# Performance work log

Hardware: AMD Instinct MI355X
Metric: run time of the kernel (lower is better)

## Reference

```python
import jax, jax.numpy as jnp
import numpy as np

CL = 256   # context_length (global in original code)
IL = 64    # inst_length (global in original code)
PC, CH1, CH2, CH3 = 64, 128, 256, 256
CK1, CK2, CK3 = 3, 3, 3
CS1, CS2, CS3 = 1, 2, 2
CP1, CP2, CP3 = 1, 1, 1
BCH1, BCH2, BCH3 = 64, 128, 256
F1, OUT = 1024, 2
B = 2048
C3_OUT = 64 * CH3            # 16384, per __init__ formula with CL-1=255
F1_IN = C3_OUT + BCH3        # 16640


def _conv1d(x, W, b, stride, pad):
    # x: [B, Cin, L], W: [Cout, Cin, K]
    y = jax.lax.conv_general_dilated(x, W, window_strides=(stride,),
                                     padding=[(pad, pad)],
                                     dimension_numbers=("NCH", "OIH", "NCH"))
    return y + b[None, :, None]


def setup_inputs() -> dict:
    key = jax.random.key(0)
    ks = jax.random.split(key, 20)
    s = lambda *sh: 1.0 / np.sqrt(np.prod(sh[1:]))
    def w(k, *sh):
        return jax.random.normal(k, sh, dtype=jnp.float32) * s(*sh)
    return {
        "x": jax.random.normal(ks[0], (B, CL * IL), dtype=jnp.float32),
        "Wp": w(ks[1], PC, IL, 2), "bp": jnp.zeros((PC,), jnp.float32),
        "W1": w(ks[2], CH1, PC, CK1), "b1": jnp.zeros((CH1,), jnp.float32),
        "W2": w(ks[3], CH2, CH1, CK2), "b2": jnp.zeros((CH2,), jnp.float32),
        "W3": w(ks[4], CH3, CH2, CK3), "b3": jnp.zeros((CH3,), jnp.float32),
        "Wb1": w(ks[5], BCH1, IL), "bb1": jnp.zeros((BCH1,), jnp.float32),
        "Wb2": w(ks[6], BCH2, BCH1), "bb2": jnp.zeros((BCH2,), jnp.float32),
        "Wb3": w(ks[7], BCH3, BCH2), "bb3": jnp.zeros((BCH3,), jnp.float32),
        "Wfc1": w(ks[8], F1, F1_IN), "bfc1": jnp.zeros((F1,), jnp.float32),
        "Wfc2": w(ks[9], OUT, F1), "bfc2": jnp.zeros((OUT,), jnp.float32),
    }


def reference(x, Wp, bp, W1, b1, W2, b2, W3, b3,
              Wb1, bb1, Wb2, bb2, Wb3, bb3, Wfc1, bfc1, Wfc2, bfc2):
    xr = x.reshape(-1, CL, IL).transpose(0, 2, 1)   # [B, IL, CL]
    x0 = xr[:, :, 0]                                 # [B, IL]
    # Fused replacement for the convp loop: kernel-2 conv over (x0, x_i)
    # y[:, :, i-1] = Wp[:,:,0] @ x0 + Wp[:,:,1] @ x_i + bp
    y = (jnp.einsum("bi,pi->bp", x0, Wp[:, :, 0])[:, :, None]
         + jnp.einsum("bic,pi->bpc", xr[:, :, 1:], Wp[:, :, 1])
         + bp[None, :, None])                        # [B, PC, CL-1]
    # bypass path on the first instruction (kernel-size-1 convs == matmuls)
    f = jax.nn.relu(x0 @ Wb1.T + bb1)
    f = jax.nn.relu(f @ Wb2.T + bb2)
    f = jax.nn.relu(f @ Wb3.T + bb3)                 # [B, BCH3]
    h = jax.nn.relu(y)
    h = jax.nn.relu(_conv1d(h, W1, b1, CS1, CP1))
    h = jax.nn.relu(_conv1d(h, W2, b2, CS2, CP2))
    h = jax.nn.relu(_conv1d(h, W3, b3, CS3, CP3))    # [B, CH3, 64]
    h = h.reshape(h.shape[0], C3_OUT)
    z = jnp.concatenate([h, f], axis=1)              # [B, F1_IN]
    z = jax.nn.relu(z @ Wfc1.T + bfc1)
    return z @ Wfc2.T + bfc2                         # [B, OUT]
```

## Files before the change

kernel.cpp:

```cpp
#include <hip/hip_runtime.h>
#include <cstdint>
#include <cstddef>

typedef __attribute__((ext_vector_type(8))) short bf16x8;
typedef __attribute__((ext_vector_type(8))) unsigned short ushort8;
typedef __attribute__((ext_vector_type(4))) float f32x4;

__device__ __forceinline__ unsigned short f2bf(float f){
  unsigned int u = __float_as_uint(f);
  unsigned int lsb = (u >> 16) & 1u;
  u += 0x7fffu + lsb;
  return (unsigned short)(u >> 16);
}

__device__ __forceinline__ void gload16(const void* g, void* l){
  __builtin_amdgcn_global_load_lds(
      (const __attribute__((address_space(1))) unsigned int*)g,
      (__attribute__((address_space(3))) unsigned int*)l, 16, 0, 0);
}

__global__ __launch_bounds__(256) void pack_w_bf16_kernel(const float* __restrict__ W,
                                                          unsigned short* __restrict__ Wb,
                                                          int COUT, int CIN){
  int idx = blockIdx.x*256 + threadIdx.x;
  int tot = COUT*CIN*3;
  if (idx >= tot) return;
  int o = idx/(CIN*3); int r = idx - o*(CIN*3); int kk = r/CIN; int ci = r - kk*CIN;
  Wb[idx] = f2bf(W[(o*CIN + ci)*3 + kk]);
}

__global__ __launch_bounds__(256) void pack_wp_kernel(const float* __restrict__ Wp,
                                                      unsigned short* __restrict__ Bw){
  int idx = blockIdx.x*256 + threadIdx.x;
  if (idx >= 64*128) return;
  int p = idx >> 7, k = idx & 127;
  float v = (k < 64) ? Wp[p*128 + k*2] : Wp[p*128 + (k-64)*2 + 1];
  Bw[idx] = f2bf(v);
}

__global__ __launch_bounds__(256) void f2bf_kernel(const float* __restrict__ src,
                                                   unsigned short* __restrict__ dst, int n){
  int i = blockIdx.x*256 + threadIdx.x;
  if (i < n) dst[i] = f2bf(src[i]);
}

__global__ __launch_bounds__(256) void zero_guards_kernel(unsigned short* __restrict__ buf,
                                                          int LINP, int CIN, int nb){
  int idx = blockIdx.x*256 + threadIdx.x;
  int per = 2*CIN/8;
  if (idx >= nb*per) return;
  int b = idx / per, r = idx - b*per;
  int g = r / (CIN/8), c8 = r - g*(CIN/8);
  ushort8 z = {0,0,0,0,0,0,0,0};
  *(ushort8*)(buf + ((size_t)b*LINP + (size_t)g*(LINP-1))*CIN + c8*8) = z;
}

__global__ __launch_bounds__(256) void branch_kernel(const float* __restrict__ x,
    const float* __restrict__ Wb1, const float* __restrict__ bb1,
    const float* __restrict__ Wb2, const float* __restrict__ bb2,
    const float* __restrict__ Wb3, const float* __restrict__ bb3,
    unsigned short* __restrict__ Hcat){
  __shared__ float s0[64], s1[64], s2[128];
  const int b = blockIdx.x, tid = threadIdx.x;
  const float* xb = x + (size_t)b*16384;
  if (tid < 64) s0[tid] = xb[tid];
  __syncthreads();
  if (tid < 64){
    float a = bb1[tid];
    for (int k=0;k<64;k++) a = fmaf(Wb1[tid*64+k], s0[k], a);
    s1[tid] = fmaxf(a, 0.f);
  }
  __syncthreads();
  if (tid < 128){
    float a = bb2[tid];
    for (int k=0;k<64;k++) a = fmaf(Wb2[tid*64+k], s1[k], a);
    s2[tid] = fmaxf(a, 0.f);
  }
  __syncthreads();
  float a = bb3[tid];
  for (int k=0;k<128;k++) a = fmaf(Wb3[tid*128+k], s2[k], a);
  Hcat[(size_t)b*16640 + 16384 + tid] = f2bf(fmaxf(a, 0.f));
}

__global__ __launch_bounds__(256) void h0_gemm_kernel(const float* __restrict__ x,
    const unsigned short* __restrict__ Bw, const float* __restrict__ bp,
    unsigned short* __restrict__ h0o){
  __shared__ __align__(16) char sAraw[128*256];
  __shared__ __align__(16) char sBraw[64*256];
  const int tid = threadIdx.x;
  const int m0 = blockIdx.x*128;
  #pragma unroll
  for (int i=0;i<16;i++){
    int j = tid + 256*i;
    int row = j >> 5, q = j & 31;
    int m = m0 + row;
    int b = m / 255, c = m - b*255;
    const float* xb = x + (size_t)b*16384;
    int k = q*4;
    const float* src = (k < 64) ? (xb + k) : (xb + (c+1)*64 + (k-64));
    float4 v = *(const float4*)src;
    ushort4 u; u.x=f2bf(v.x); u.y=f2bf(v.y); u.z=f2bf(v.z); u.w=f2bf(v.w);
    *(ushort4*)(sAraw + row*256 + ((k*2) ^ ((row&7)<<4))) = u;
  }
  #pragma unroll
  for (int i=0;i<4;i++){
    int j = tid + 256*i;
    int row = j >> 4, q = j & 15;
    int k = q*8;
    ushort8 u = *(const ushort8*)(Bw + row*128 + k);
    *(ushort8*)(sBraw + row*256 + ((k*2) ^ ((row&7)<<4))) = u;
  }
  __syncthreads();
  const int lane = tid & 63, wid = tid >> 6;
  const int lr = lane & 15, lg = lane >> 4;
  f32x4 zero = {0.f,0.f,0.f,0.f};
  f32x4 acc[2][4];
  #pragma unroll
  for (int a=0;a<2;a++){ acc[a][0]=zero; acc[a][1]=zero; acc[a][2]=zero; acc[a][3]=zero; }
  #pragma unroll
  for (int ks=0; ks<4; ks++){
    int k = ks*32 + lg*8;
    bf16x8 af[2], bfr[4];
    #pragma unroll
    for (int f=0; f<2; f++){
      int row = wid*32 + f*16 + lr;
      af[f] = *(const bf16x8*)(sAraw + row*256 + ((k*2) ^ ((row&7)<<4)));
    }
    #pragma unroll
    for (int f=0; f<4; f++){
      int row = f*16 + lr;
      bfr[f] = *(const bf16x8*)(sBraw + row*256 + ((k*2) ^ ((row&7)<<4)));
    }
    #pragma unroll
    for (int fi=0; fi<2; fi++)
      #pragma unroll
      for (int fj=0; fj<4; fj++)
        acc[fi][fj] = __builtin_amdgcn_mfma_f32_16x16x32_bf16(af[fi], bfr[fj], acc[fi][fj], 0,0,0);
  }
  #pragma unroll
  for (int fi=0; fi<2; fi++)
    #pragma unroll
    for (int fj=0; fj<4; fj++)
      #pragma unroll
      for (int j=0;j<4;j++){
        int m = m0 + wid*32 + fi*16 + lg*4 + j;
        int n = fj*16 + lr;
        int b = m / 255, t = m - b*255;
        h0o[((size_t)b*257 + t + 1)*64 + n] = f2bf(fmaxf(acc[fi][fj][j] + bp[n], 0.f));
      }
}

template<int CIN,int COUT,int S,int LINP,int LOUT,bool TO_HCAT>
__global__ __launch_bounds__(256) void conv_gemm_kernel(
    const unsigned short* __restrict__ in, const unsigned short* __restrict__ Wb,
    const float* __restrict__ bias, unsigned short* __restrict__ out){
  constexpr int K = 3*CIN;
  constexpr int KS = K/64;
  __shared__ __align__(16) char sA[128*128];
  __shared__ __align__(16) char sB[128*128];
  const int tid = threadIdx.x;
  const int m0 = blockIdx.x*128;
  const int n0 = blockIdx.y*128;
  const int lane = tid & 63, wid = tid >> 6;
  const int wm = wid >> 1, wn = wid & 1;
  const int lr = lane & 15, lg = lane >> 4;
  const int srow = lane >> 3;
  const int soff = (((lane&7) ^ srow) << 3);
  const unsigned short* abase[4];
  const unsigned short* bbase[4];
  #pragma unroll
  for (int s=0;s<4;s++){
    int row = wid*32 + s*8 + srow;
    int m = m0 + row;
    int b = m / LOUT, t = m - b*LOUT;
    abase[s] = in + ((size_t)b*LINP + (size_t)t*S)*CIN + soff;
    bbase[s] = Wb + (size_t)(n0+row)*K + soff;
  }
  f32x4 zero = {0.f,0.f,0.f,0.f};
  f32x4 acc[4][4];
  #pragma unroll
  for (int i=0;i<4;i++){ acc[i][0]=zero; acc[i][1]=zero; acc[i][2]=zero; acc[i][3]=zero; }
  for (int ks=0; ks<KS; ks++){
    const int k0 = ks*64;
    __syncthreads();
    #pragma unroll
    for (int s=0;s<4;s++){
      gload16(abase[s] + k0, sA + wid*4096 + s*1024);
      gload16(bbase[s] + k0, sB + wid*4096 + s*1024);
    }
    __syncthreads();
    #pragma unroll
    for (int kss=0; kss<2; kss++){
      const int k = kss*32 + lg*8;
      bf16x8 af[4], bfr[4];
      #pragma unroll
      for (int f=0;f<4;f++){
        int ra = wm*64 + f*16 + lr;
        af[f]  = *(const bf16x8*)(sA + ra*128 + ((k*2) ^ ((ra&7)<<4)));
        int rb = wn*64 + f*16 + lr;
        bfr[f] = *(const bf16x8*)(sB + rb*128 + ((k*2) ^ ((rb&7)<<4)));
      }
      #pragma unroll
      for (int fi=0;fi<4;fi++)
        #pragma unroll
        for (int fj=0;fj<4;fj++)
          acc[fi][fj] = __builtin_amdgcn_mfma_f32_16x16x32_bf16(af[fi], bfr[fj], acc[fi][fj], 0,0,0);
    }
  }
  #pragma unroll
  for (int fi=0;fi<4;fi++)
    #pragma unroll
    for (int fj=0;fj<4;fj++)
      #pragma unroll
      for (int j=0;j<4;j++){
        int m = m0 + wm*64 + fi*16 + lg*4 + j;
        int n = n0 + wn*64 + fj*16 + lr;
        int b = m / LOUT, t = m - b*LOUT;
        float val = fmaxf(acc[fi][fj][j] + bias[n], 0.f);
        if (TO_HCAT) out[(size_t)b*16640 + (size_t)n*64 + t] = f2bf(val);
        else         out[((size_t)b*(LOUT+2) + t + 1)*COUT + n] = f2bf(val);
      }
}

__global__ __launch_bounds__(256) void fc1_gemm_kernel(
    const unsigned short* __restrict__ A, const unsigned short* __restrict__ Bw,
    float* __restrict__ zp, int zoffm, int MT, int KZ){
  __shared__ __align__(16) char sA[128*128];
  __shared__ __align__(16) char sB[128*128];
  const int tid = threadIdx.x;
  const int nwg = gridDim.x;
  const int lgid = (blockIdx.x % 8)*(nwg/8) + blockIdx.x/8;
  const int kz  = lgid / (8*MT);
  const int rem = lgid % (8*MT);
  const int nt  = rem / MT;
  const int mt  = rem % MT;
  const int n0 = nt*128, m0 = mt*128;
  const int lane = tid & 63, wid = tid >> 6;
  const int wm = wid >> 1, wn = wid & 1;
  const int lr = lane & 15, lg = lane >> 4;
  const int srow = lane >> 3;
  const int soff = (((lane&7) ^ srow) << 3);
  f32x4 zero = {0.f,0.f,0.f,0.f};
  f32x4 acc[4][4];
  #pragma unroll
  for (int i=0;i<4;i++){ acc[i][0]=zero; acc[i][1]=zero; acc[i][2]=zero; acc[i][3]=zero; }
  const int it0 = (kz*260)/KZ, it1 = ((kz+1)*260)/KZ;
  for (int it=it0; it<it1; ++it){
    const size_t k0 = (size_t)it*64;
    __syncthreads();
    #pragma unroll
    for (int s=0;s<4;s++){
      int row = wid*32 + s*8 + srow;
      gload16(A  + (size_t)(m0+row)*16640 + k0 + soff, sA + wid*4096 + s*1024);
      gload16(Bw + (size_t)(n0+row)*16640 + k0 + soff, sB + wid*4096 + s*1024);
    }
    __syncthreads();
    #pragma unroll
    for (int ks=0; ks<2; ks++){
      const int k = ks*32 + lg*8;
      bf16x8 af[4], bfr[4];
      #pragma unroll
      for (int f=0;f<4;f++){
        int rowa = wm*64 + f*16 + lr;
        af[f]  = *(const bf16x8*)(sA + rowa*128 + ((k*2) ^ ((rowa&7)<<4)));
        int rowb = wn*64 + f*16 + lr;
        bfr[f] = *(const bf16x8*)(sB + rowb*128 + ((k*2) ^ ((rowb&7)<<4)));
      }
      #pragma unroll
      for (int fi=0;fi<4;fi++)
        #pragma unroll
        for (int fj=0;fj<4;fj++)
          acc[fi][fj] = __builtin_amdgcn_mfma_f32_16x16x32_bf16(af[fi], bfr[fj], acc[fi][fj], 0,0,0);
    }
  }
  float* zo = zp + (size_t)kz*zoffm;
  #pragma unroll
  for (int fi=0;fi<4;fi++)
    #pragma unroll
    for (int fj=0;fj<4;fj++)
      #pragma unroll
      for (int j=0;j<4;j++){
        int m = m0 + wm*64 + fi*16 + lg*4 + j;
        int n = n0 + wn*64 + fj*16 + lr;
        zo[(size_t)m*1024 + n] = acc[fi][fj][j];
      }
}

__global__ __launch_bounds__(256) void fc2_kernel(const float* __restrict__ zp, int zoffm, int KZ,
    const float* __restrict__ bfc1, const float* __restrict__ Wfc2,
    const float* __restrict__ bfc2, float* __restrict__ out){
  __shared__ float red[4][2];
  const int b = blockIdx.x, tid = threadIdx.x;
  float a0 = 0.f, a1 = 0.f;
  for (int n = tid; n < 1024; n += 256){
    float s = bfc1[n];
    const float* zb = zp + (size_t)b*1024 + n;
    for (int kz = 0; kz < KZ; kz++) s += zb[(size_t)kz*zoffm];
    s = fmaxf(s, 0.f);
    a0 = fmaf(s, Wfc2[n], a0);
    a1 = fmaf(s, Wfc2[1024+n], a1);
  }
  #pragma unroll
  for (int m=32; m>=1; m>>=1){ a0 += __shfl_xor(a0, m, 64); a1 += __shfl_xor(a1, m, 64); }
  const int w = tid >> 6;
  if ((tid & 63) == 0){ red[w][0] = a0; red[w][1] = a1; }
  __syncthreads();
  if (tid == 0){
    float s0 = red[0][0]+red[1][0]+red[2][0]+red[3][0];
    float s1 = red[0][1]+red[1][1]+red[2][1]+red[3][1];
    out[(size_t)b*2]   = s0 + bfc2[0];
    out[(size_t)b*2+1] = s1 + bfc2[1];
  }
}

extern "C" void kernel_launch(void* const* d_in, const int* in_sizes, int n_in,
                              void* d_out, int out_size, void* d_ws, size_t ws_size,
                              hipStream_t stream){
  const float* x    = (const float*)d_in[0];
  const float* Wp   = (const float*)d_in[1];
  const float* bp   = (const float*)d_in[2];
  const float* W1   = (const float*)d_in[3];
  const float* b1   = (const float*)d_in[4];
  const float* W2   = (const float*)d_in[5];
  const float* b2   = (const float*)d_in[6];
  const float* W3   = (const float*)d_in[7];
  const float* b3   = (const float*)d_in[8];
  const float* Wb1  = (const float*)d_in[9];
  const float* bb1  = (const float*)d_in[10];
  const float* Wb2  = (const float*)d_in[11];
  const float* bb2  = (const float*)d_in[12];
  const float* Wb3  = (const float*)d_in[13];
  const float* bb3  = (const float*)d_in[14];
  const float* Wfc1 = (const float*)d_in[15];
  const float* bfc1 = (const float*)d_in[16];
  const float* Wfc2 = (const float*)d_in[17];
  const float* bfc2 = (const float*)d_in[18];
  float* out = (float*)d_out;

  size_t off = 0;
  char* basep = (char*)d_ws;
  auto carve = [&](size_t bytes)->char*{
    char* q = basep + off; off += (bytes + 255) & ~(size_t)255; return q;
  };
  unsigned short* W1b   = (unsigned short*)carve((size_t)128*3*64*2);
  unsigned short* W2b   = (unsigned short*)carve((size_t)256*3*128*2);
  unsigned short* W3b   = (unsigned short*)carve((size_t)256*3*256*2);
  unsigned short* Bwp   = (unsigned short*)carve((size_t)64*128*2);
  unsigned short* Wfc1b = (unsigned short*)carve((size_t)1024*16640*2);
  size_t fixed = off;

  int Bc = 128, KZ = 64;
  {
    const int bcs[5] = {2048, 1024, 512, 256, 128};
    const int kzs[5] = {4, 8, 16, 32, 64};
    for (int i = 0; i < 5; i++){
      size_t b = bcs[i];
      size_t need = fixed + b*((size_t)66560+65792+33280) + (size_t)kzs[i]*b*4096 + 16*256;
      if (need <= ws_size){ Bc = bcs[i]; KZ = kzs[i]; break; }
    }
  }
  const int NC = 2048/Bc;
  const int MT = Bc/128;
  unsigned short* buf1 = (unsigned short*)carve((size_t)Bc*66560);
  unsigned short* buf2 = (unsigned short*)carve((size_t)Bc*65792);
  unsigned short* Hcat = (unsigned short*)carve((size_t)Bc*33280);
  float*          zp   = (float*)carve((size_t)KZ*Bc*4096);
  const int zoffm = Bc*1024;

  hipLaunchKernelGGL(pack_w_bf16_kernel, dim3((128*64*3+255)/256), dim3(256), 0, stream, W1, W1b, 128, 64);
  hipLaunchKernelGGL(pack_w_bf16_kernel, dim3((256*128*3+255)/256), dim3(256), 0, stream, W2, W2b, 256, 128);
  hipLaunchKernelGGL(pack_w_bf16_kernel, dim3((256*256*3+255)/256), dim3(256), 0, stream, W3, W3b, 256, 256);
  hipLaunchKernelGGL(pack_wp_kernel, dim3(32), dim3(256), 0, stream, Wp, Bwp);
  hipLaunchKernelGGL(f2bf_kernel, dim3((17039360+255)/256), dim3(256), 0, stream, Wfc1, Wfc1b, 17039360);

  for (int c = 0; c < NC; ++c){
    const float* xc = x + (size_t)c*Bc*16384;
    hipLaunchKernelGGL(zero_guards_kernel, dim3((Bc*2*64/8+255)/256), dim3(256), 0, stream,
                       buf1, 257, 64, Bc);
    hipLaunchKernelGGL(zero_guards_kernel, dim3((Bc*2*128/8+255)/256), dim3(256), 0, stream,
                       buf2, 257, 128, Bc);
    hipLaunchKernelGGL(branch_kernel, dim3(Bc), dim3(256), 0, stream,
                       xc, Wb1, bb1, Wb2, bb2, Wb3, bb3, Hcat);
    hipLaunchKernelGGL(h0_gemm_kernel, dim3(Bc*255/128), dim3(256), 0, stream, xc, Bwp, bp, buf1);
    hipLaunchKernelGGL((conv_gemm_kernel<64,128,1,257,255,false>), dim3(Bc*255/128, 1), dim3(256), 0, stream,
                       buf1, W1b, b1, buf2);
    hipLaunchKernelGGL(zero_guards_kernel, dim3((Bc*2*256/8+255)/256), dim3(256), 0, stream,
                       buf1, 130, 256, Bc);
    hipLaunchKernelGGL((conv_gemm_kernel<128,256,2,257,128,false>), dim3(Bc, 2), dim3(256), 0, stream,
                       buf2, W2b, b2, buf1);
    hipLaunchKernelGGL((conv_gemm_kernel<256,256,2,130,64,true>), dim3(Bc/2, 2), dim3(256), 0, stream,
                       buf1, W3b, b3, Hcat);
    hipLaunchKernelGGL(fc1_gemm_kernel, dim3(8*MT*KZ), dim3(256), 0, stream,
                       Hcat, Wfc1b, zp, zoffm, MT, KZ);
    hipLaunchKernelGGL(fc2_kernel, dim3(Bc), dim3(256), 0, stream,
                       zp, zoffm, KZ, bfc1, Wfc2, bfc2, out + (size_t)c*Bc*2);
  }
}
```

Measured before the change: 554.8 us.

## Replace conv im2col GEMM with per-sample slab-staged conv kernels

The three conv layers now load a contiguous slab of input rows for one sample into LDS once and reuse it across the three kernel taps, instead of re-gathering an im2col-style A tile for every K chunk. Weight tiles are double-buffered so the next chunk's load overlaps the current MFMAs, and a swizzled block index remaps workgroups. Buffers are split into separate h0/c1/c2 areas so all guard zeroing happens up front. The trade-off is smaller M tiles for conv2 and conv3 (64 and 32 rows), which lowers MFMA work per block and adds more blocks.

```diff
diff --git a/kernel.cpp b/kernel.cpp
--- a/kernel.cpp
+++ b/kernel.cpp
@@ -20,8 +20,7 @@
 }
 
 __global__ __launch_bounds__(256) void pack_w_bf16_kernel(const float* __restrict__ W,
-                                                          unsigned short* __restrict__ Wb,
-                                                          int COUT, int CIN){
+    unsigned short* __restrict__ Wb, int COUT, int CIN){
   int idx = blockIdx.x*256 + threadIdx.x;
   int tot = COUT*CIN*3;
   if (idx >= tot) return;
@@ -113,10 +112,11 @@
   __syncthreads();
   const int lane = tid & 63, wid = tid >> 6;
   const int lr = lane & 15, lg = lane >> 4;
-  f32x4 zero = {0.f,0.f,0.f,0.f};
   f32x4 acc[2][4];
   #pragma unroll
-  for (int a=0;a<2;a++){ acc[a][0]=zero; acc[a][1]=zero; acc[a][2]=zero; acc[a][3]=zero; }
+  for (int a=0;a<2;a++)
+    #pragma unroll
+    for (int j=0;j<4;j++) acc[a][j] = (f32x4){0,0,0,0};
   #pragma unroll
   for (int ks=0; ks<4; ks++){
     int k = ks*32 + lg*8;
@@ -150,75 +150,109 @@
       }
 }
 
-template<int CIN,int COUT,int S,int LINP,int LOUT,bool TO_HCAT>
-__global__ __launch_bounds__(256) void conv_gemm_kernel(
+template<int CIN,int COUT,int S,int LOUT,int PADIN,int PADOUT,int BM,int MPB,int MF,bool TO_HCAT>
+__global__ __launch_bounds__(256) void conv_slab_kernel(
     const unsigned short* __restrict__ in, const unsigned short* __restrict__ Wb,
     const float* __restrict__ bias, unsigned short* __restrict__ out){
-  constexpr int K = 3*CIN;
-  constexpr int KS = K/64;
-  __shared__ __align__(16) char sA[128*128];
-  __shared__ __align__(16) char sB[128*128];
-  const int tid = threadIdx.x;
-  const int m0 = blockIdx.x*128;
-  const int n0 = blockIdx.y*128;
-  const int lane = tid & 63, wid = tid >> 6;
-  const int wm = wid >> 1, wn = wid & 1;
-  const int lr = lane & 15, lg = lane >> 4;
-  const int srow = lane >> 3;
-  const int soff = (((lane&7) ^ srow) << 3);
-  const unsigned short* abase[4];
-  const unsigned short* bbase[4];
-  #pragma unroll
-  for (int s=0;s<4;s++){
-    int row = wid*32 + s*8 + srow;
-    int m = m0 + row;
-    int b = m / LOUT, t = m - b*LOUT;
-    abase[s] = in + ((size_t)b*LINP + (size_t)t*S)*CIN + soff;
-    bbase[s] = Wb + (size_t)(n0+row)*K + soff;
-  }
-  f32x4 zero = {0.f,0.f,0.f,0.f};
-  f32x4 acc[4][4];
-  #pragma unroll
-  for (int i=0;i<4;i++){ acc[i][0]=zero; acc[i][1]=zero; acc[i][2]=zero; acc[i][3]=zero; }
-  for (int ks=0; ks<KS; ks++){
-    const int k0 = ks*64;
-    __syncthreads();
+  constexpr int NT   = COUT/128;
+  constexpr int NCH  = 3*CIN/64;
+  constexpr int CP8  = CIN/8;
+  constexpr int CB   = CIN*2;
+  constexpr int SROWS = 2048/CP8;
+  constexpr int LDSROWS = SROWS + 4;
+  __shared__ __align__(16) char S_[LDSROWS*CB + 32768];
+  char* SA = S_;
+  char* SB = S_ + LDSROWS*CB;
+
+  const int tid = threadIdx.x, lane = tid & 63, wv = tid >> 6;
+  const int nwg = gridDim.x;
+  const int bid = blockIdx.x;
+  const int lgid = (bid & 7)*(nwg >> 3) + (bid >> 3);
+  const int nt  = lgid % NT;
+  const int mtb = lgid / NT;
+  const int mt  = mtb % MPB;
+  const int b   = mtb / MPB;
+  const int n0  = nt*128;
+  const int t0  = mt*BM;
+  const unsigned short* Ab = in + ((size_t)b*PADIN + (size_t)t0*S)*CIN;
+
+  #pragma unroll
+  for (int i=0;i<8;i++){
+    int slot = (wv*8+i)*64 + lane;
+    int row = slot / CP8, p = slot % CP8;
+    gload16(Ab + (size_t)row*CIN + ((p ^ ((row>>1)&7))<<3), SA + (wv*8+i)*1024);
+  }
+  if (wv == 0 && lane < CP8){
+    int row = SROWS, p = lane;
+    gload16(Ab + (size_t)row*CIN + ((p ^ ((row>>1)&7))<<3), SA + SROWS*CB);
+  }
+  if (tid < 3*CP8){
+    int r = SROWS + 1 + tid/CP8, p = tid%CP8;
+    *(ushort8*)(SA + r*CB + p*16) = (ushort8){0,0,0,0,0,0,0,0};
+  }
+
+  const int brow = lane >> 3, bp8 = lane & 7;
+  auto stageB = [&](int c, int bufi){
     #pragma unroll
     for (int s=0;s<4;s++){
-      gload16(abase[s] + k0, sA + wid*4096 + s*1024);
-      gload16(bbase[s] + k0, sB + wid*4096 + s*1024);
-    }
-    __syncthreads();
-    #pragma unroll
-    for (int kss=0; kss<2; kss++){
-      const int k = kss*32 + lg*8;
-      bf16x8 af[4], bfr[4];
+      int row = wv*32 + s*8 + brow;
+      gload16(Wb + (size_t)(n0+row)*(3*CIN) + c*64 + ((bp8 ^ (row&7))<<3),
+              SB + bufi*16384 + wv*4096 + s*1024);
+    }
+  };
+  stageB(0, 0);
+  __syncthreads();
+
+  const int wm = wv>>1, wn = wv&1;
+  const int lr = lane&15, lg = lane>>4;
+  f32x4 acc[MF][4];
+  #pragma unroll
+  for (int i=0;i<MF;i++)
+    #pragma unroll
+    for (int j=0;j<4;j++) acc[i][j] = (f32x4){0,0,0,0};
+
+  int buf = 0;
+  #pragma unroll
+  for (int c=0;c<NCH;c++){
+    if (c+1 < NCH) stageB(c+1, buf^1);
+    const int kk = c/(CIN/64), cc = c%(CIN/64);
+    #pragma unroll
+    for (int ks=0; ks<2; ks++){
+      bf16x8 af[MF], bfr[4];
+      #pragma unroll
+      for (int f=0;f<MF;f++){
+        int row = (wm*(BM/2) + f*16 + lr)*S + kk;
+        int ci = cc*8 + ks*4 + lg;
+        af[f] = *(const bf16x8*)(SA + row*CB + ((ci ^ ((row>>1)&7))<<4));
+      }
       #pragma unroll
       for (int f=0;f<4;f++){
-        int ra = wm*64 + f*16 + lr;
-        af[f]  = *(const bf16x8*)(sA + ra*128 + ((k*2) ^ ((ra&7)<<4)));
         int rb = wn*64 + f*16 + lr;
-        bfr[f] = *(const bf16x8*)(sB + rb*128 + ((k*2) ^ ((rb&7)<<4)));
-      }
-      #pragma unroll
-      for (int fi=0;fi<4;fi++)
+        bfr[f] = *(const bf16x8*)(SB + buf*16384 + rb*128 + (((ks*4+lg) ^ (rb&7))<<4));
+      }
+      #pragma unroll
+      for (int fi=0;fi<MF;fi++)
         #pragma unroll
         for (int fj=0;fj<4;fj++)
           acc[fi][fj] = __builtin_amdgcn_mfma_f32_16x16x32_bf16(af[fi], bfr[fj], acc[fi][fj], 0,0,0);
     }
-  }
-  #pragma unroll
-  for (int fi=0;fi<4;fi++)
+    __syncthreads();
+    buf ^= 1;
+  }
+
+  #pragma unroll
+  for (int fi=0;fi<MF;fi++)
     #pragma unroll
     for (int fj=0;fj<4;fj++)
       #pragma unroll
       for (int j=0;j<4;j++){
-        int m = m0 + wm*64 + fi*16 + lg*4 + j;
+        int t = wm*(BM/2) + fi*16 + lg*4 + j;
         int n = n0 + wn*64 + fj*16 + lr;
-        int b = m / LOUT, t = m - b*LOUT;
-        float val = fmaxf(acc[fi][fj][j] + bias[n], 0.f);
-        if (TO_HCAT) out[(size_t)b*16640 + (size_t)n*64 + t] = f2bf(val);
-        else         out[((size_t)b*(LOUT+2) + t + 1)*COUT + n] = f2bf(val);
+        if (BM <= LOUT || t < LOUT){
+          float v = fmaxf(acc[fi][fj][j] + bias[n], 0.f);
+          if (TO_HCAT) out[(size_t)b*16640 + (size_t)n*64 + (t0 + t)] = f2bf(v);
+          else         out[((size_t)b*PADOUT + t0 + t + 1)*COUT + n] = f2bf(v);
+        }
       }
 }
 
@@ -240,10 +274,11 @@
   const int lr = lane & 15, lg = lane >> 4;
   const int srow = lane >> 3;
   const int soff = (((lane&7) ^ srow) << 3);
-  f32x4 zero = {0.f,0.f,0.f,0.f};
   f32x4 acc[4][4];
   #pragma unroll
-  for (int i=0;i<4;i++){ acc[i][0]=zero; acc[i][1]=zero; acc[i][2]=zero; acc[i][3]=zero; }
+  for (int i=0;i<4;i++)
+    #pragma unroll
+    for (int j=0;j<4;j++) acc[i][j] = (f32x4){0,0,0,0};
   const int it0 = (kz*260)/KZ, it1 = ((kz+1)*260)/KZ;
   for (int it=it0; it<it1; ++it){
     const size_t k0 = (size_t)it*64;
@@ -306,10 +341,8 @@
   if ((tid & 63) == 0){ red[w][0] = a0; red[w][1] = a1; }
   __syncthreads();
   if (tid == 0){
-    float s0 = red[0][0]+red[1][0]+red[2][0]+red[3][0];
-    float s1 = red[0][1]+red[1][1]+red[2][1]+red[3][1];
-    out[(size_t)b*2]   = s0 + bfc2[0];
-    out[(size_t)b*2+1] = s1 + bfc2[1];
+    out[(size_t)b*2]   = red[0][0]+red[1][0]+red[2][0]+red[3][0] + bfc2[0];
+    out[(size_t)b*2+1] = red[0][1]+red[1][1]+red[2][1]+red[3][1] + bfc2[1];
   }
 }
 
@@ -354,15 +387,16 @@
     const int bcs[5] = {2048, 1024, 512, 256, 128};
     const int kzs[5] = {4, 8, 16, 32, 64};
     for (int i = 0; i < 5; i++){
-      size_t b = bcs[i];
-      size_t need = fixed + b*((size_t)66560+65792+33280) + (size_t)kzs[i]*b*4096 + 16*256;
+      size_t bsz = bcs[i];
+      size_t need = fixed + bsz*((size_t)32896+65792+66560+33280) + (size_t)kzs[i]*bsz*4096 + 64*256;
       if (need <= ws_size){ Bc = bcs[i]; KZ = kzs[i]; break; }
     }
   }
   const int NC = 2048/Bc;
   const int MT = Bc/128;
-  unsigned short* buf1 = (unsigned short*)carve((size_t)Bc*66560);
-  unsigned short* buf2 = (unsigned short*)carve((size_t)Bc*65792);
+  unsigned short* h0p  = (unsigned short*)carve((size_t)Bc*32896);
+  unsigned short* c1p  = (unsigned short*)carve((size_t)Bc*65792);
+  unsigned short* c2p  = (unsigned short*)carve((size_t)Bc*66560);
   unsigned short* Hcat = (unsigned short*)carve((size_t)Bc*33280);
   float*          zp   = (float*)carve((size_t)KZ*Bc*4096);
   const int zoffm = Bc*1024;
@@ -375,21 +409,18 @@
 
   for (int c = 0; c < NC; ++c){
     const float* xc = x + (size_t)c*Bc*16384;
-    hipLaunchKernelGGL(zero_guards_kernel, dim3((Bc*2*64/8+255)/256), dim3(256), 0, stream,
-                       buf1, 257, 64, Bc);
-    hipLaunchKernelGGL(zero_guards_kernel, dim3((Bc*2*128/8+255)/256), dim3(256), 0, stream,
-                       buf2, 257, 128, Bc);
+    hipLaunchKernelGGL(zero_guards_kernel, dim3((Bc*2*64/8+255)/256), dim3(256), 0, stream, h0p, 257, 64, Bc);
+    hipLaunchKernelGGL(zero_guards_kernel, dim3((Bc*2*128/8+255)/256), dim3(256), 0, stream, c1p, 257, 128, Bc);
+    hipLaunchKernelGGL(zero_guards_kernel, dim3((Bc*2*256/8+255)/256), dim3(256), 0, stream, c2p, 130, 256, Bc);
     hipLaunchKernelGGL(branch_kernel, dim3(Bc), dim3(256), 0, stream,
                        xc, Wb1, bb1, Wb2, bb2, Wb3, bb3, Hcat);
-    hipLaunchKernelGGL(h0_gemm_kernel, dim3(Bc*255/128), dim3(256), 0, stream, xc, Bwp, bp, buf1);
-    hipLaunchKernelGGL((conv_gemm_kernel<64,128,1,257,255,false>), dim3(Bc*255/128, 1), dim3(256), 0, stream,
-                       buf1, W1b, b1, buf2);
-    hipLaunchKernelGGL(zero_guards_kernel, dim3((Bc*2*256/8+255)/256), dim3(256), 0, stream,
-                       buf1, 130, 256, Bc);
-    hipLaunchKernelGGL((conv_gemm_kernel<128,256,2,257,128,false>), dim3(Bc, 2), dim3(256), 0, stream,
-                       buf2, W2b, b2, buf1);
-    hipLaunchKernelGGL((conv_gemm_kernel<256,256,2,130,64,true>), dim3(Bc/2, 2), dim3(256), 0, stream,
-                       buf1, W3b, b3, Hcat);
+    hipLaunchKernelGGL(h0_gemm_kernel, dim3(Bc*255/128), dim3(256), 0, stream, xc, Bwp, bp, h0p);
+    hipLaunchKernelGGL((conv_slab_kernel<64,128,1,255,257,257,256,1,8,false>),
+                       dim3(Bc), dim3(256), 0, stream, h0p, W1b, b1, c1p);
+    hipLaunchKernelGGL((conv_slab_kernel<128,256,2,128,257,130,64,2,2,false>),
+                       dim3(Bc*4), dim3(256), 0, stream, c1p, W2b, b2, c2p);
+    hipLaunchKernelGGL((conv_slab_kernel<256,256,2,64,130,0,32,2,1,true>),
+                       dim3(Bc*4), dim3(256), 0, stream, c2p, W3b, b3, Hcat);
     hipLaunchKernelGGL(fc1_gemm_kernel, dim3(8*MT*KZ), dim3(256), 0, stream,
                        Hcat, Wfc1b, zp, zoffm, MT, KZ);
     hipLaunchKernelGGL(fc2_kernel, dim3(Bc), dim3(256), 0, stream,
```

Result: slower. 588.8 us (+6.1%).

## Double-buffer LDS tiles in conv and fc1 GEMMs, swizzle conv block order

Applied to the files above, without the earlier changes.

The conv and fc1 GEMM kernels now use two LDS buffers: the global-to-LDS loads for the next K-step are issued before the MFMA work on the current step, with one barrier per iteration instead of two. The conv kernel also remaps block indices in groups of eight so consecutive tiles spread across XCDs, and its K loop is fully unrolled. The aim is to hide global load latency behind matrix math. In exchange, LDS per block doubles to 64KB, which may lower occupancy. Correctness relies on the barrier waiting for the asynchronous LDS loads to finish.

```diff
diff --git a/kernel.cpp b/kernel.cpp
--- a/kernel.cpp
+++ b/kernel.cpp
@@ -20,8 +20,7 @@
 }
 
 __global__ __launch_bounds__(256) void pack_w_bf16_kernel(const float* __restrict__ W,
-                                                          unsigned short* __restrict__ Wb,
-                                                          int COUT, int CIN){
+    unsigned short* __restrict__ Wb, int COUT, int CIN){
   int idx = blockIdx.x*256 + threadIdx.x;
   int tot = COUT*CIN*3;
   if (idx >= tot) return;
@@ -113,10 +112,11 @@
   __syncthreads();
   const int lane = tid & 63, wid = tid >> 6;
   const int lr = lane & 15, lg = lane >> 4;
-  f32x4 zero = {0.f,0.f,0.f,0.f};
   f32x4 acc[2][4];
   #pragma unroll
-  for (int a=0;a<2;a++){ acc[a][0]=zero; acc[a][1]=zero; acc[a][2]=zero; acc[a][3]=zero; }
+  for (int a=0;a<2;a++)
+    #pragma unroll
+    for (int j=0;j<4;j++) acc[a][j] = (f32x4){0,0,0,0};
   #pragma unroll
   for (int ks=0; ks<4; ks++){
     int k = ks*32 + lg*8;
@@ -156,10 +156,15 @@
     const float* __restrict__ bias, unsigned short* __restrict__ out){
   constexpr int K = 3*CIN;
   constexpr int KS = K/64;
-  __shared__ __align__(16) char sA[128*128];
-  __shared__ __align__(16) char sB[128*128];
+  __shared__ __align__(16) char sA[2*128*128];
+  __shared__ __align__(16) char sB[2*128*128];
   const int tid = threadIdx.x;
-  const int m0 = blockIdx.x*128;
+  int m0;
+  {
+    int bid = blockIdx.x, nwg = gridDim.x;
+    if ((nwg & 7) == 0){ int q = nwg >> 3; m0 = ((bid & 7)*q + (bid >> 3))*128; }
+    else m0 = bid*128;
+  }
   const int n0 = blockIdx.y*128;
   const int lane = tid & 63, wid = tid >> 6;
   const int wm = wid >> 1, wn = wid & 1;
@@ -176,19 +181,26 @@
     abase[s] = in + ((size_t)b*LINP + (size_t)t*S)*CIN + soff;
     bbase[s] = Wb + (size_t)(n0+row)*K + soff;
   }
-  f32x4 zero = {0.f,0.f,0.f,0.f};
   f32x4 acc[4][4];
   #pragma unroll
-  for (int i=0;i<4;i++){ acc[i][0]=zero; acc[i][1]=zero; acc[i][2]=zero; acc[i][3]=zero; }
+  for (int i=0;i<4;i++)
+    #pragma unroll
+    for (int j=0;j<4;j++) acc[i][j] = (f32x4){0,0,0,0};
+
+  auto stage = [&](int ks, int bufi){
+    const int k0 = ks*64;
+    #pragma unroll
+    for (int s=0;s<4;s++){
+      gload16(abase[s] + k0, sA + bufi*16384 + wid*4096 + s*1024);
+      gload16(bbase[s] + k0, sB + bufi*16384 + wid*4096 + s*1024);
+    }
+  };
+  stage(0, 0);
+  __syncthreads();
+  int buf = 0;
+  #pragma unroll
   for (int ks=0; ks<KS; ks++){
-    const int k0 = ks*64;
-    __syncthreads();
-    #pragma unroll
-    for (int s=0;s<4;s++){
-      gload16(abase[s] + k0, sA + wid*4096 + s*1024);
-      gload16(bbase[s] + k0, sB + wid*4096 + s*1024);
-    }
-    __syncthreads();
+    if (ks+1 < KS) stage(ks+1, buf^1);
     #pragma unroll
     for (int kss=0; kss<2; kss++){
       const int k = kss*32 + lg*8;
@@ -196,9 +208,9 @@
       #pragma unroll
       for (int f=0;f<4;f++){
         int ra = wm*64 + f*16 + lr;
-        af[f]  = *(const bf16x8*)(sA + ra*128 + ((k*2) ^ ((ra&7)<<4)));
+        af[f]  = *(const bf16x8*)(sA + buf*16384 + ra*128 + ((k*2) ^ ((ra&7)<<4)));
         int rb = wn*64 + f*16 + lr;
-        bfr[f] = *(const bf16x8*)(sB + rb*128 + ((k*2) ^ ((rb&7)<<4)));
+        bfr[f] = *(const bf16x8*)(sB + buf*16384 + rb*128 + ((k*2) ^ ((rb&7)<<4)));
       }
       #pragma unroll
       for (int fi=0;fi<4;fi++)
@@ -206,6 +218,8 @@
         for (int fj=0;fj<4;fj++)
           acc[fi][fj] = __builtin_amdgcn_mfma_f32_16x16x32_bf16(af[fi], bfr[fj], acc[fi][fj], 0,0,0);
     }
+    __syncthreads();
+    buf ^= 1;
   }
   #pragma unroll
   for (int fi=0;fi<4;fi++)
@@ -225,8 +239,8 @@
 __global__ __launch_bounds__(256) void fc1_gemm_kernel(
     const unsigned short* __restrict__ A, const unsigned short* __restrict__ Bw,
     float* __restrict__ zp, int zoffm, int MT, int KZ){
-  __shared__ __align__(16) char sA[128*128];
-  __shared__ __align__(16) char sB[128*128];
+  __shared__ __align__(16) char sA[2*128*128];
+  __shared__ __align__(16) char sB[2*128*128];
   const int tid = threadIdx.x;
   const int nwg = gridDim.x;
   const int lgid = (blockIdx.x % 8)*(nwg/8) + blockIdx.x/8;
@@ -240,21 +254,27 @@
   const int lr = lane & 15, lg = lane >> 4;
   const int srow = lane >> 3;
   const int soff = (((lane&7) ^ srow) << 3);
-  f32x4 zero = {0.f,0.f,0.f,0.f};
   f32x4 acc[4][4];
   #pragma unroll
-  for (int i=0;i<4;i++){ acc[i][0]=zero; acc[i][1]=zero; acc[i][2]=zero; acc[i][3]=zero; }
+  for (int i=0;i<4;i++)
+    #pragma unroll
+    for (int j=0;j<4;j++) acc[i][j] = (f32x4){0,0,0,0};
   const int it0 = (kz*260)/KZ, it1 = ((kz+1)*260)/KZ;
-  for (int it=it0; it<it1; ++it){
+
+  auto stage = [&](int it, int bufi){
     const size_t k0 = (size_t)it*64;
-    __syncthreads();
     #pragma unroll
     for (int s=0;s<4;s++){
       int row = wid*32 + s*8 + srow;
-      gload16(A  + (size_t)(m0+row)*16640 + k0 + soff, sA + wid*4096 + s*1024);
-      gload16(Bw + (size_t)(n0+row)*16640 + k0 + soff, sB + wid*4096 + s*1024);
-    }
-    __syncthreads();
+      gload16(A  + (size_t)(m0+row)*16640 + k0 + soff, sA + bufi*16384 + wid*4096 + s*1024);
+      gload16(Bw + (size_t)(n0+row)*16640 + k0 + soff, sB + bufi*16384 + wid*4096 + s*1024);
+    }
+  };
+  stage(it0, 0);
+  __syncthreads();
+  int buf = 0;
+  for (int it=it0; it<it1; ++it){
+    if (it+1 < it1) stage(it+1, buf^1);
     #pragma unroll
     for (int ks=0; ks<2; ks++){
       const int k = ks*32 + lg*8;
@@ -262,9 +282,9 @@
       #pragma unroll
       for (int f=0;f<4;f++){
         int rowa = wm*64 + f*16 + lr;
-        af[f]  = *(const bf16x8*)(sA + rowa*128 + ((k*2) ^ ((rowa&7)<<4)));
+        af[f]  = *(const bf16x8*)(sA + buf*16384 + rowa*128 + ((k*2) ^ ((rowa&7)<<4)));
         int rowb = wn*64 + f*16 + lr;
-        bfr[f] = *(const bf16x8*)(sB + rowb*128 + ((k*2) ^ ((rowb&7)<<4)));
+        bfr[f] = *(const bf16x8*)(sB + buf*16384 + rowb*128 + ((k*2) ^ ((rowb&7)<<4)));
       }
       #pragma unroll
       for (int fi=0;fi<4;fi++)
@@ -272,6 +292,8 @@
         for (int fj=0;fj<4;fj++)
           acc[fi][fj] = __builtin_amdgcn_mfma_f32_16x16x32_bf16(af[fi], bfr[fj], acc[fi][fj], 0,0,0);
     }
+    __syncthreads();
+    buf ^= 1;
   }
   float* zo = zp + (size_t)kz*zoffm;
   #pragma unroll
@@ -306,10 +328,8 @@
   if ((tid & 63) == 0){ red[w][0] = a0; red[w][1] = a1; }
   __syncthreads();
   if (tid == 0){
-    float s0 = red[0][0]+red[1][0]+red[2][0]+red[3][0];
-    float s1 = red[0][1]+red[1][1]+red[2][1]+red[3][1];
-    out[(size_t)b*2]   = s0 + bfc2[0];
-    out[(size_t)b*2+1] = s1 + bfc2[1];
+    out[(size_t)b*2]   = red[0][0]+red[1][0]+red[2][0]+red[3][0] + bfc2[0];
+    out[(size_t)b*2+1] = red[0][1]+red[1][1]+red[2][1]+red[3][1] + bfc2[1];
   }
 }
 
```

After: 547.5 us. About the same (-1.3%).
